# Optimization experiments

Measured on AMD Instinct MI355X. Metric: run time of the kernel, lower is better.

## Reference

```python
import jax, jax.numpy as jnp
import numpy as np

D_IN = 4096
D_OUT = 4096
TOKENS = 8192


def setup_inputs() -> dict:
    key = jax.random.key(0)
    k_x, k_w = jax.random.split(key)
    x = jax.random.normal(k_x, (TOKENS, D_IN), dtype=jnp.float32)
    # int8 weight buffer (stored as int32 for jax friendliness; values in [-128,127))
    weight_i8 = jax.random.randint(k_w, (D_OUT, D_IN), -128, 127, dtype=jnp.int32)
    return {
        "x": x,
        "weight_i8": weight_i8,
        "weight_scale": jnp.array([0.01], dtype=jnp.float32),
        "weight_zero_point": jnp.zeros((1,), dtype=jnp.int32),
        "bias": jnp.zeros((D_OUT,), dtype=jnp.float32),
        "output_scale": jnp.array([0.5], dtype=jnp.float32),
        "output_zero_point": jnp.full((1,), 128, dtype=jnp.int32),
    }


def reference(x, weight_i8, weight_scale, weight_zero_point, bias,
              output_scale, output_zero_point):
    # NOTE: the torch module also computes torch.quantize_per_tensor(x, ...)
    # whose result is unused (dead code); it does not affect the output and
    # is omitted here.
    # Dequantize int8 weight: (w_int - zp) * scale  -> [D_OUT, D_IN] fp32
    w = (weight_i8.astype(jnp.float32)
         - weight_zero_point.astype(jnp.float32)) * weight_scale
    # Standard fp32 linear: [T, D_IN] @ [D_IN, D_OUT] + bias
    out = jnp.einsum("ti,oi->to", x, w) + bias
    # quantize_per_tensor(out, output_scale, output_zp, quint8).dequantize():
    # q = clamp(round(out/scale) + zp, 0, 255); deq = (q - zp) * scale
    zp = output_zero_point.astype(jnp.float32)
    q = jnp.clip(jnp.round(out / output_scale) + zp, 0.0, 255.0)
    return (q - zp) * output_scale
```

## Files before the change

### kernel.cpp

```cpp
#include <hip/hip_runtime.h>

#define TOKENS 8192
#define D_IN   4096
#define D_OUT  4096

typedef _Float16 f16;
typedef __attribute__((ext_vector_type(8))) _Float16 half8;
typedef __attribute__((ext_vector_type(4))) float    f32x4;
typedef __attribute__((address_space(3))) char       lds_char;


__global__ void cvt_x_kernel(const float* __restrict__ x, f16* __restrict__ xh) {
    size_t i = ((size_t)blockIdx.x * blockDim.x + threadIdx.x) * 4;
    float4 v = *reinterpret_cast<const float4*>(x + i);
    union { f16 h[4]; uint2 u; } p;
    p.h[0] = (f16)v.x; p.h[1] = (f16)v.y; p.h[2] = (f16)v.z; p.h[3] = (f16)v.w;
    *reinterpret_cast<uint2*>(xh + i) = p.u;
}

__global__ void cvt_w_kernel(const int* __restrict__ w, f16* __restrict__ wh,
                             const float* __restrict__ scale_p,
                             const int* __restrict__ zp_p) {
    size_t i = ((size_t)blockIdx.x * blockDim.x + threadIdx.x) * 4;
    float s = scale_p[0];
    float z = (float)zp_p[0];
    int4 v = *reinterpret_cast<const int4*>(w + i);
    union { f16 h[4]; uint2 u; } p;
    p.h[0] = (f16)(((float)v.x - z) * s);
    p.h[1] = (f16)(((float)v.y - z) * s);
    p.h[2] = (f16)(((float)v.z - z) * s);
    p.h[3] = (f16)(((float)v.w - z) * s);
    *reinterpret_cast<uint2*>(wh + i) = p.u;
}


#define BM 256
#define BN 256
#define BK 32
#define NT (D_IN / BK)
#define BUFSZ 32768
#define B_OFF 16384

__device__ __forceinline__ void stage16(const f16* g, lds_char* l) {
    __builtin_amdgcn_global_load_lds(
        (const __attribute__((address_space(1))) void*)g,
        (__attribute__((address_space(3))) void*)l, 16, 0, 0);
}

#define LDS_LOAD8(p) (*(const __attribute__((address_space(3))) half8*)(p))

#define BAR()      __builtin_amdgcn_s_barrier()
#define VMCNT(N)   asm volatile("s_waitcnt vmcnt(" #N ")" ::: "memory")
#define PRIO(x)    __builtin_amdgcn_s_setprio(x)

#define READS_AND_MFMA(BUF)                                                 \
    do {                                                                    \
        _Pragma("unroll")                                                   \
        for (int fm = 0; fm < 8; ++fm)                                      \
            a[fm] = LDS_LOAD8((BUF) + aoff + fm * 1024);                    \
        _Pragma("unroll")                                                   \
        for (int fn = 0; fn < 4; ++fn)                                      \
            b[fn] = LDS_LOAD8((BUF) + boff + fn * 1024);                    \
        PRIO(1);                                                            \
        _Pragma("unroll")                                                   \
        for (int fm = 0; fm < 8; ++fm)                                      \
            _Pragma("unroll")                                               \
            for (int fn = 0; fn < 4; ++fn)                                  \
                acc[fm][fn] = __builtin_amdgcn_mfma_f32_16x16x32_f16(       \
                    a[fm], b[fn], acc[fm][fn], 0, 0, 0);                    \
        PRIO(0);                                                            \
    } while (0)

#define STAGE_TILE(TT)                                                      \
    do {                                                                    \
        lds_char* dst = dstbase + ((TT) & 3) * BUFSZ;                       \
        const f16* sA = gA + (size_t)(TT) * BK;                             \
        const f16* sB = gB + (size_t)(TT) * BK;                             \
        stage16(sA,                    dst);                                \
        stage16(sA + (size_t)128 * K,  dst + 8192);                         \
        stage16(sB,                    dst + B_OFF);                        \
        stage16(sB + (size_t)128 * K,  dst + B_OFF + 8192);                 \
    } while (0)

__global__ __launch_bounds__(512, 2)
void gemm_dp(const f16* __restrict__ A, const f16* __restrict__ B,
             const float* __restrict__ bias,
             const float* __restrict__ oscale_p, const int* __restrict__ ozp_p,
             float* __restrict__ C)
{
    __shared__ __align__(1024) char smem_[4 * BUFSZ];
    lds_char* smem = (lds_char*)smem_;
    constexpr int K = D_IN, N = D_OUT;

    int nwg = gridDim.x;
    int cpx = nwg >> 3;
    int bid = blockIdx.x;
    int swz = (bid & 7) * cpx + (bid >> 3);
    int ntn = N / BN;
    int m0 = (swz / ntn) * BM;
    int n0 = (swz % ntn) * BN;

    int tid = threadIdx.x;
    int l   = tid & 63;
    int wv  = tid >> 6;
    int wr  = wv >> 2;
    int wc  = wv & 3;
    int lr  = l & 15;

    int srow = wv * 16 + (l >> 2);
    int scol = ((l & 3) ^ ((srow >> 1) & 3)) * 8;
    const f16* gA = A + (size_t)(m0 + srow) * K + scol;
    const f16* gB = B + (size_t)(n0 + srow) * K + scol;
    lds_char* dstbase = smem + wv * 1024 + l * 16;

    int colsel = ((l >> 4) ^ ((lr >> 1) & 3)) << 4;
    int aoff = (wr * 128 + lr) * 64 + colsel;
    int boff = B_OFF + (wc * 64 + lr) * 64 + colsel;

    f32x4 acc[8][4] = {};
    half8 a[8], b[4];

    STAGE_TILE(0);
    STAGE_TILE(1);
    STAGE_TILE(2);
    VMCNT(8);
    BAR();

    for (int t = 0; t < NT - 3; ++t) {
        const lds_char* buf = smem + (t & 3) * BUFSZ;
        STAGE_TILE(t + 3);
        READS_AND_MFMA(buf);
        VMCNT(8);
        BAR();
    }
    {
        READS_AND_MFMA(smem + ((NT - 3) & 3) * BUFSZ);
        VMCNT(4);
        BAR();
        READS_AND_MFMA(smem + ((NT - 2) & 3) * BUFSZ);
        VMCNT(0);
        BAR();
        READS_AND_MFMA(smem + ((NT - 1) & 3) * BUFSZ);
    }

    float os  = oscale_p[0];
    float ozp = (float)ozp_p[0];
    float inv = 1.0f / os;
    #pragma unroll
    for (int fm = 0; fm < 8; ++fm) {
        int rowb = m0 + wr * 128 + fm * 16 + (l >> 4) * 4;
        #pragma unroll
        for (int fn = 0; fn < 4; ++fn) {
            int col = n0 + wc * 64 + fn * 16 + lr;
            float bv = bias[col];
            f32x4 v = acc[fm][fn];
            #pragma unroll
            for (int j = 0; j < 4; ++j) {
                float o = v[j] + bv;
                float q = rintf(o * inv) + ozp;
                q = fminf(fmaxf(q, 0.0f), 255.0f);
                C[(size_t)(rowb + j) * N + col] = (q - ozp) * os;
            }
        }
    }
}


extern "C" void kernel_launch(void* const* d_in, const int* in_sizes, int n_in,
                              void* d_out, int out_size, void* d_ws, size_t ws_size,
                              hipStream_t stream) {
    const float* x      = (const float*)d_in[0];
    const int*   w8     = (const int*)d_in[1];
    const float* wscale = (const float*)d_in[2];
    const int*   wzp    = (const int*)d_in[3];
    const float* bias   = (const float*)d_in[4];
    const float* oscale = (const float*)d_in[5];
    const int*   ozp    = (const int*)d_in[6];
    float* out = (float*)d_out;

    const size_t x_elems = (size_t)TOKENS * D_IN;
    const size_t w_elems = (size_t)D_OUT * D_IN;
    const size_t need = (x_elems + w_elems) * sizeof(f16);
    if (ws_size < need) return;

    f16* xh = (f16*)d_ws;
    f16* wh = xh + x_elems;

    {
        int blocks = (int)(x_elems / 4 / 256);
        cvt_x_kernel<<<blocks, 256, 0, stream>>>(x, xh);
    }
    {
        int blocks = (int)(w_elems / 4 / 256);
        cvt_w_kernel<<<blocks, 256, 0, stream>>>(w8, wh, wscale, wzp);
    }
    {
        int grid = (TOKENS / BM) * (D_OUT / BN);
        gemm_dp<<<grid, 512, 0, stream>>>(xh, wh, bias, oscale, ozp, out);
    }
}
```

Before: 292.4 us.

## Double-buffer LDS fragment reads in registers to overlap with MFMA

Splits the per-tile LDS reads and MFMA block into separate steps and keeps two register banks of A/B fragments (even and odd). The loop is unrolled by two so that the fragments of tile t+1 are read from LDS while the MFMAs for tile t run, and the prologue and epilogue are adjusted to match. The goal is to hide LDS read latency behind matrix math, at the cost of roughly doubling the fragment registers, which risks spills or lower occupancy under the 512x2 launch bounds.

```diff
diff --git a/kernel.cpp b/kernel.cpp
--- a/kernel.cpp
+++ b/kernel.cpp
@@ -53,24 +53,6 @@
 #define VMCNT(N)   asm volatile("s_waitcnt vmcnt(" #N ")" ::: "memory")
 #define PRIO(x)    __builtin_amdgcn_s_setprio(x)
 
-#define READS_AND_MFMA(BUF)                                                 \
-    do {                                                                    \
-        _Pragma("unroll")                                                   \
-        for (int fm = 0; fm < 8; ++fm)                                      \
-            a[fm] = LDS_LOAD8((BUF) + aoff + fm * 1024);                    \
-        _Pragma("unroll")                                                   \
-        for (int fn = 0; fn < 4; ++fn)                                      \
-            b[fn] = LDS_LOAD8((BUF) + boff + fn * 1024);                    \
-        PRIO(1);                                                            \
-        _Pragma("unroll")                                                   \
-        for (int fm = 0; fm < 8; ++fm)                                      \
-            _Pragma("unroll")                                               \
-            for (int fn = 0; fn < 4; ++fn)                                  \
-                acc[fm][fn] = __builtin_amdgcn_mfma_f32_16x16x32_f16(       \
-                    a[fm], b[fn], acc[fm][fn], 0, 0, 0);                    \
-        PRIO(0);                                                            \
-    } while (0)
-
 #define STAGE_TILE(TT)                                                      \
     do {                                                                    \
         lds_char* dst = dstbase + ((TT) & 3) * BUFSZ;                       \
@@ -82,8 +64,31 @@
         stage16(sB + (size_t)128 * K,  dst + B_OFF + 8192);                 \
     } while (0)
 
+#define READ_BANK(AB, BB, TREAD)                                            \
+    do {                                                                    \
+        const lds_char* rbuf = smem + ((TREAD) & 3) * BUFSZ;                \
+        _Pragma("unroll")                                                   \
+        for (int fm = 0; fm < 8; ++fm)                                      \
+            AB[fm] = LDS_LOAD8(rbuf + aoff + fm * 1024);                    \
+        _Pragma("unroll")                                                   \
+        for (int fn = 0; fn < 4; ++fn)                                      \
+            BB[fn] = LDS_LOAD8(rbuf + boff + fn * 1024);                    \
+    } while (0)
+
+#define MFMA_BANK(AB, BB)                                                   \
+    do {                                                                    \
+        PRIO(1);                                                            \
+        _Pragma("unroll")                                                   \
+        for (int fm = 0; fm < 8; ++fm)                                      \
+            _Pragma("unroll")                                               \
+            for (int fn = 0; fn < 4; ++fn)                                  \
+                acc[fm][fn] = __builtin_amdgcn_mfma_f32_16x16x32_f16(       \
+                    a##AB[fm], b##BB[fn], acc[fm][fn], 0, 0, 0);            \
+        PRIO(0);                                                            \
+    } while (0)
+
 __global__ __launch_bounds__(512, 2)
-void gemm_dp(const f16* __restrict__ A, const f16* __restrict__ B,
+void gemm_xb(const f16* __restrict__ A, const f16* __restrict__ B,
              const float* __restrict__ bias,
              const float* __restrict__ oscale_p, const int* __restrict__ ozp_p,
              float* __restrict__ C)
@@ -118,29 +123,42 @@
     int boff = B_OFF + (wc * 64 + lr) * 64 + colsel;
 
     f32x4 acc[8][4] = {};
-    half8 a[8], b[4];
+    half8 aE[8], bE[4], aO[8], bO[4];
 
     STAGE_TILE(0);
     STAGE_TILE(1);
+    VMCNT(4);
+    BAR();
+    READ_BANK(aE, bE, 0);
     STAGE_TILE(2);
-    VMCNT(8);
+    VMCNT(4);
     BAR();
 
-    for (int t = 0; t < NT - 3; ++t) {
-        const lds_char* buf = smem + (t & 3) * BUFSZ;
+    for (int t = 0; t < NT - 4; t += 2) {
         STAGE_TILE(t + 3);
-        READS_AND_MFMA(buf);
-        VMCNT(8);
-        BAR();
-    }
-    {
-        READS_AND_MFMA(smem + ((NT - 3) & 3) * BUFSZ);
+        READ_BANK(aO, bO, t + 1);
+        MFMA_BANK(E, E);
         VMCNT(4);
         BAR();
-        READS_AND_MFMA(smem + ((NT - 2) & 3) * BUFSZ);
+        STAGE_TILE(t + 4);
+        READ_BANK(aE, bE, t + 2);
+        MFMA_BANK(O, O);
+        VMCNT(4);
+        BAR();
+    }
+    {
+        STAGE_TILE(NT - 1);
+        READ_BANK(aO, bO, NT - 3);
+        MFMA_BANK(E, E);
+        VMCNT(4);
+        BAR();
+        READ_BANK(aE, bE, NT - 2);
+        MFMA_BANK(O, O);
         VMCNT(0);
         BAR();
-        READS_AND_MFMA(smem + ((NT - 1) & 3) * BUFSZ);
+        READ_BANK(aO, bO, NT - 1);
+        MFMA_BANK(E, E);
+        MFMA_BANK(O, O);
     }
 
     float os  = oscale_p[0];
@@ -196,6 +214,6 @@
     }
     {
         int grid = (TOKENS / BM) * (D_OUT / BN);
-        gemm_dp<<<grid, 512, 0, stream>>>(xh, wh, bias, oscale, ozp, out);
-    }
-}
+        gemm_xb<<<grid, 512, 0, stream>>>(xh, wh, bias, oscale, ozp, out);
+    }
+}
```

New measurement: 292.1 us. Within noise of the previous version (-0.1%).
